# Performance work log

Hardware: AMD Instinct MI355X
Metric: run time of the kernel (lower is better)

## Reference

```python
import jax, jax.numpy as jnp
import numpy as np

B, I, O = 2048, 512, 512

def setup_inputs() -> dict:
    key = jax.random.key(0)
    kx, kw, ks = jax.random.split(key, 3)
    x = jax.random.uniform(kx, (B, I), dtype=jnp.float32)
    # shift weight logits so sigmoid(w) ~ 0.02: keeps the length-I product
    # of implication factors away from underflow (sparse conjunction)
    w_logits = jax.random.normal(kw, (I, O), dtype=jnp.float32) - 4.0
    s_logits = jax.random.normal(ks, (I, O), dtype=jnp.float32)
    return {"x": x, "w_logits": w_logits, "s_logits": s_logits}

def reference(x, w_logits, s_logits):
    # FuzzyParam.value(): sigmoid of stored logits
    w = jax.nn.sigmoid(w_logits)   # (I, O)
    s = jax.nn.sigmoid(s_logits)   # (I, O)
    xi = x[:, :, None]             # (B, I, 1)
    # product fuzzy logic:
    #   bin_xnor(a, b) = a*b + (1-a)*(1-b)
    #   implies(a, b)  = 1 - a*(1 - b)
    #   conjoin        = prod along axis
    xnor = xi * s + (1.0 - xi) * (1.0 - s)      # (B, I, O)
    factors = 1.0 - w * (1.0 - xnor)            # (B, I, O)
    return jnp.prod(factors, axis=1)            # (B, O)
```

## Files before the change

kernel.cpp:

```cpp
#include <hip/hip_runtime.h>
#include <hip/hip_bf16.h>
#include <math.h>

#define B_DIM 2048
#define I_DIM 512
#define O_DIM 512

constexpr int R_ROWS  = 8;
constexpr int W_CHUNK = 4;
constexpr int CHUNK   = I_DIM / W_CHUNK;
constexpr int KP      = CHUNK / 2;
constexpr int QUADS   = I_DIM / 4;

#define XT_BYTES  ((size_t)B_DIM * I_DIM * 4)
#define AB_OFFSET XT_BYTES

__global__ __launch_bounds__(256) void setup_kernel(
    const float* __restrict__ x,
    const float* __restrict__ w_logits,
    const float* __restrict__ s_logits,
    float4* __restrict__ ab4,
    float4* __restrict__ xt4)
{
    const int blk = blockIdx.x;
    if (blk < 512) {
        int t = blk * 256 + threadIdx.x;
        int o  = t & (O_DIM - 1);
        int k  = t >> 9;
        int i0 = 2 * k;

        float zw0 = w_logits[(i0 + 0) * O_DIM + o];
        float zs0 = s_logits[(i0 + 0) * O_DIM + o];
        float zw1 = w_logits[(i0 + 1) * O_DIM + o];
        float zs1 = s_logits[(i0 + 1) * O_DIM + o];

        float w0 = 1.0f / (1.0f + expf(-zw0));
        float s0 = 1.0f / (1.0f + expf(-zs0));
        float w1 = 1.0f / (1.0f + expf(-zw1));
        float s1 = 1.0f / (1.0f + expf(-zs1));

        float4 v;
        v.x = fmaf(-w0, s0, 1.0f);
        v.y = fmaf(-w1, s1, 1.0f);
        v.z = w0 * (2.0f * s0 - 1.0f);
        v.w = w1 * (2.0f * s1 - 1.0f);
        ab4[k * O_DIM + o] = v;
    } else {
        int t  = (blk - 512) * 256 + threadIdx.x;
        int q  = t & (QUADS - 1);
        int b  = t >> 7;
        float4 v = ((const float4*)x)[(size_t)b * QUADS + q];
        xt4[((size_t)(b >> 3) * QUADS + q) * R_ROWS + (b & 7)] = v;
    }
}

__global__ __launch_bounds__(1024, 8) void fuzzy_main(
    const float4* __restrict__ xt,
    const float4* __restrict__ ab4,
    float* __restrict__ out)
{
    __shared__ float part[W_CHUNK][R_ROWS][256];

    const int o_l = threadIdx.x;
    const int o   = blockIdx.x * 256 + o_l;
    const int y   = __builtin_amdgcn_readfirstlane((int)threadIdx.y);
    const int g   = blockIdx.y;
    const int b0  = g * R_ROWS;
    const int kbase = y * KP;

    const float4* ab_o = ab4 + o;
    const float4* xq = xt + ((size_t)g * QUADS + (size_t)y * (KP / 2)) * R_ROWS;

    float4 xa[R_ROWS], xb[R_ROWS];
#pragma unroll
    for (int r = 0; r < R_ROWS; ++r) xa[r] = xq[r];
#pragma unroll
    for (int r = 0; r < R_ROWS; ++r) xb[r] = xq[R_ROWS + r];

    float4 pA0 = ab_o[(size_t)(kbase + 0) * O_DIM];
    float4 pA1 = ab_o[(size_t)(kbase + 1) * O_DIM];
    float4 pB0 = ab_o[(size_t)(kbase + 2) * O_DIM];
    float4 pB1 = ab_o[(size_t)(kbase + 3) * O_DIM];

    float acc0[R_ROWS], acc1[R_ROWS];
#pragma unroll
    for (int r = 0; r < R_ROWS; ++r) { acc0[r] = 1.0f; acc1[r] = 1.0f; }

    for (int k = 0; k < KP; k += 4) {
        {
            float4 c0 = pA0, c1 = pA1;
#pragma unroll
            for (int r = 0; r < R_ROWS; ++r) {
                float4 xv = xa[r];
                float f0 = fmaf(c0.z, xv.x, c0.x);
                float f1 = fmaf(c0.w, xv.y, c0.y);
                float f2 = fmaf(c1.z, xv.z, c1.x);
                float f3 = fmaf(c1.w, xv.w, c1.y);
                acc0[r] *= f0 * f2;
                acc1[r] *= f1 * f3;
            }
            pA0 = ab_o[(size_t)(kbase + k + 4) * O_DIM];
            pA1 = ab_o[(size_t)(kbase + k + 5) * O_DIM];
            const float4* xs = xq + (size_t)(k / 2 + 2) * R_ROWS;
#pragma unroll
            for (int r = 0; r < R_ROWS; ++r) xa[r] = xs[r];
        }
        {
            float4 c0 = pB0, c1 = pB1;
#pragma unroll
            for (int r = 0; r < R_ROWS; ++r) {
                float4 xv = xb[r];
                float f0 = fmaf(c0.z, xv.x, c0.x);
                float f1 = fmaf(c0.w, xv.y, c0.y);
                float f2 = fmaf(c1.z, xv.z, c1.x);
                float f3 = fmaf(c1.w, xv.w, c1.y);
                acc0[r] *= f0 * f2;
                acc1[r] *= f1 * f3;
            }
            pB0 = ab_o[(size_t)(kbase + k + 6) * O_DIM];
            pB1 = ab_o[(size_t)(kbase + k + 7) * O_DIM];
            const float4* xs = xq + (size_t)(k / 2 + 3) * R_ROWS;
#pragma unroll
            for (int r = 0; r < R_ROWS; ++r) xb[r] = xs[r];
        }
    }

#pragma unroll
    for (int r = 0; r < R_ROWS; ++r)
        part[y][r][o_l] = acc0[r] * acc1[r];
    __syncthreads();
#pragma unroll
    for (int rr = 0; rr < 2; ++rr) {
        int r8 = y * 2 + rr;
        float v = part[0][r8][o_l] * part[1][r8][o_l]
                * part[2][r8][o_l] * part[3][r8][o_l];
        out[(size_t)(b0 + r8) * O_DIM + o] = v;
    }
}

extern "C" void kernel_launch(void* const* d_in, const int* in_sizes, int n_in,
                              void* d_out, int out_size, void* d_ws, size_t ws_size,
                              hipStream_t stream) {
    const float* x        = (const float*)d_in[0];
    const float* w_logits = (const float*)d_in[1];
    const float* s_logits = (const float*)d_in[2];
    float* out = (float*)d_out;
    float4* xt4 = (float4*)d_ws;
    float4* ab4 = (float4*)((char*)d_ws + AB_OFFSET);

    setup_kernel<<<dim3(1536), dim3(256), 0, stream>>>(
        x, w_logits, s_logits, ab4, xt4);

    fuzzy_main<<<dim3(O_DIM / 256, B_DIM / R_ROWS), dim3(256, W_CHUNK), 0, stream>>>(
        xt4, ab4, out);
}
```

Baseline: 92.73 us.

## Stage x rows in LDS and double rows per block, drop x transpose pass

Removes the x-transpose half of the setup kernel and instead has each block cooperatively load its 16 rows of x into shared memory, which is then reused for the final partial-product reduction. Rows per block go from 8 to 16, halving the grid and doubling reuse of each loaded weight-coefficient vector. The two accumulators per row are merged into one. This trades a global transpose pass and per-thread register-held x for LDS broadcast reads plus an extra barrier, with lower occupancy hints.

```diff
diff --git a/kernel.cpp b/kernel.cpp
--- a/kernel.cpp
+++ b/kernel.cpp
@@ -1,65 +1,52 @@
 #include <hip/hip_runtime.h>
-#include <hip/hip_bf16.h>
 #include <math.h>
 
 #define B_DIM 2048
 #define I_DIM 512
 #define O_DIM 512
 
-constexpr int R_ROWS  = 8;
+constexpr int R_ROWS  = 16;
 constexpr int W_CHUNK = 4;
 constexpr int CHUNK   = I_DIM / W_CHUNK;
 constexpr int KP      = CHUNK / 2;
-constexpr int QUADS   = I_DIM / 4;
 
-#define XT_BYTES  ((size_t)B_DIM * I_DIM * 4)
-#define AB_OFFSET XT_BYTES
 
 __global__ __launch_bounds__(256) void setup_kernel(
-    const float* __restrict__ x,
     const float* __restrict__ w_logits,
     const float* __restrict__ s_logits,
-    float4* __restrict__ ab4,
-    float4* __restrict__ xt4)
+    float4* __restrict__ ab4)
 {
-    const int blk = blockIdx.x;
-    if (blk < 512) {
-        int t = blk * 256 + threadIdx.x;
-        int o  = t & (O_DIM - 1);
-        int k  = t >> 9;
-        int i0 = 2 * k;
+    int t  = blockIdx.x * 256 + threadIdx.x;
+    int o  = t & (O_DIM - 1);
+    int k  = t >> 9;
+    int i0 = 2 * k;
 
-        float zw0 = w_logits[(i0 + 0) * O_DIM + o];
-        float zs0 = s_logits[(i0 + 0) * O_DIM + o];
-        float zw1 = w_logits[(i0 + 1) * O_DIM + o];
-        float zs1 = s_logits[(i0 + 1) * O_DIM + o];
+    float zw0 = w_logits[(i0 + 0) * O_DIM + o];
+    float zs0 = s_logits[(i0 + 0) * O_DIM + o];
+    float zw1 = w_logits[(i0 + 1) * O_DIM + o];
+    float zs1 = s_logits[(i0 + 1) * O_DIM + o];
 
-        float w0 = 1.0f / (1.0f + expf(-zw0));
-        float s0 = 1.0f / (1.0f + expf(-zs0));
-        float w1 = 1.0f / (1.0f + expf(-zw1));
-        float s1 = 1.0f / (1.0f + expf(-zs1));
+    float w0 = 1.0f / (1.0f + expf(-zw0));
+    float s0 = 1.0f / (1.0f + expf(-zs0));
+    float w1 = 1.0f / (1.0f + expf(-zw1));
+    float s1 = 1.0f / (1.0f + expf(-zs1));
 
-        float4 v;
-        v.x = fmaf(-w0, s0, 1.0f);
-        v.y = fmaf(-w1, s1, 1.0f);
-        v.z = w0 * (2.0f * s0 - 1.0f);
-        v.w = w1 * (2.0f * s1 - 1.0f);
-        ab4[k * O_DIM + o] = v;
-    } else {
-        int t  = (blk - 512) * 256 + threadIdx.x;
-        int q  = t & (QUADS - 1);
-        int b  = t >> 7;
-        float4 v = ((const float4*)x)[(size_t)b * QUADS + q];
-        xt4[((size_t)(b >> 3) * QUADS + q) * R_ROWS + (b & 7)] = v;
-    }
+    float4 v;
+    v.x = fmaf(-w0, s0, 1.0f);
+    v.y = fmaf(-w1, s1, 1.0f);
+    v.z = w0 * (2.0f * s0 - 1.0f);
+    v.w = w1 * (2.0f * s1 - 1.0f);
+    ab4[k * O_DIM + o] = v;
 }
 
-__global__ __launch_bounds__(1024, 8) void fuzzy_main(
-    const float4* __restrict__ xt,
+__global__ __launch_bounds__(1024, 4) void fuzzy_main(
+    const float* __restrict__ x,
     const float4* __restrict__ ab4,
     float* __restrict__ out)
 {
-    __shared__ float part[W_CHUNK][R_ROWS][256];
+    __shared__ __align__(16) unsigned char sh_raw[W_CHUNK * R_ROWS * 256 * 4];
+    float4 (*xs4)[CHUNK]        = reinterpret_cast<float4(*)[CHUNK]>(sh_raw);
+    float  (*part)[R_ROWS][256] = reinterpret_cast<float(*)[R_ROWS][256]>(sh_raw);
 
     const int o_l = threadIdx.x;
     const int o   = blockIdx.x * 256 + o_l;
@@ -69,72 +56,72 @@
     const int kbase = y * KP;
 
     const float4* ab_o = ab4 + o;
-    const float4* xq = xt + ((size_t)g * QUADS + (size_t)y * (KP / 2)) * R_ROWS;
-
-    float4 xa[R_ROWS], xb[R_ROWS];
-#pragma unroll
-    for (int r = 0; r < R_ROWS; ++r) xa[r] = xq[r];
-#pragma unroll
-    for (int r = 0; r < R_ROWS; ++r) xb[r] = xq[R_ROWS + r];
 
     float4 pA0 = ab_o[(size_t)(kbase + 0) * O_DIM];
     float4 pA1 = ab_o[(size_t)(kbase + 1) * O_DIM];
     float4 pB0 = ab_o[(size_t)(kbase + 2) * O_DIM];
     float4 pB1 = ab_o[(size_t)(kbase + 3) * O_DIM];
 
-    float acc0[R_ROWS], acc1[R_ROWS];
+    {
+        const float4* x4 = (const float4*)x;
+        const int tid = threadIdx.y * 256 + o_l;
 #pragma unroll
-    for (int r = 0; r < R_ROWS; ++r) { acc0[r] = 1.0f; acc1[r] = 1.0f; }
+        for (int p = 0; p < 2; ++p) {
+            int fidx = p * 1024 + tid;
+            int r = fidx >> 7;
+            int q = fidx & (CHUNK - 1);
+            xs4[r][q] = x4[(size_t)(b0 + r) * (I_DIM / 4) + q];
+        }
+    }
+    __syncthreads();
+
+    float acc[R_ROWS];
+#pragma unroll
+    for (int r = 0; r < R_ROWS; ++r) acc[r] = 1.0f;
 
     for (int k = 0; k < KP; k += 4) {
+        const int qA = (kbase + k) >> 1;
         {
             float4 c0 = pA0, c1 = pA1;
+            pA0 = ab_o[(size_t)(kbase + k + 4) * O_DIM];
+            pA1 = ab_o[(size_t)(kbase + k + 5) * O_DIM];
 #pragma unroll
             for (int r = 0; r < R_ROWS; ++r) {
-                float4 xv = xa[r];
+                float4 xv = xs4[r][qA];
                 float f0 = fmaf(c0.z, xv.x, c0.x);
                 float f1 = fmaf(c0.w, xv.y, c0.y);
                 float f2 = fmaf(c1.z, xv.z, c1.x);
                 float f3 = fmaf(c1.w, xv.w, c1.y);
-                acc0[r] *= f0 * f2;
-                acc1[r] *= f1 * f3;
+                acc[r] *= (f0 * f2) * (f1 * f3);
             }
-            pA0 = ab_o[(size_t)(kbase + k + 4) * O_DIM];
-            pA1 = ab_o[(size_t)(kbase + k + 5) * O_DIM];
-            const float4* xs = xq + (size_t)(k / 2 + 2) * R_ROWS;
-#pragma unroll
-            for (int r = 0; r < R_ROWS; ++r) xa[r] = xs[r];
         }
         {
             float4 c0 = pB0, c1 = pB1;
+            pB0 = ab_o[(size_t)(kbase + k + 6) * O_DIM];
+            pB1 = ab_o[(size_t)(kbase + k + 7) * O_DIM];
 #pragma unroll
             for (int r = 0; r < R_ROWS; ++r) {
-                float4 xv = xb[r];
+                float4 xv = xs4[r][qA + 1];
                 float f0 = fmaf(c0.z, xv.x, c0.x);
                 float f1 = fmaf(c0.w, xv.y, c0.y);
                 float f2 = fmaf(c1.z, xv.z, c1.x);
                 float f3 = fmaf(c1.w, xv.w, c1.y);
-                acc0[r] *= f0 * f2;
-                acc1[r] *= f1 * f3;
+                acc[r] *= (f0 * f2) * (f1 * f3);
             }
-            pB0 = ab_o[(size_t)(kbase + k + 6) * O_DIM];
-            pB1 = ab_o[(size_t)(kbase + k + 7) * O_DIM];
-            const float4* xs = xq + (size_t)(k / 2 + 3) * R_ROWS;
-#pragma unroll
-            for (int r = 0; r < R_ROWS; ++r) xb[r] = xs[r];
         }
     }
 
+    __syncthreads();
 #pragma unroll
     for (int r = 0; r < R_ROWS; ++r)
-        part[y][r][o_l] = acc0[r] * acc1[r];
+        part[y][r][o_l] = acc[r];
     __syncthreads();
 #pragma unroll
-    for (int rr = 0; rr < 2; ++rr) {
-        int r8 = y * 2 + rr;
-        float v = part[0][r8][o_l] * part[1][r8][o_l]
-                * part[2][r8][o_l] * part[3][r8][o_l];
-        out[(size_t)(b0 + r8) * O_DIM + o] = v;
+    for (int rr = 0; rr < 4; ++rr) {
+        int r = y * 4 + rr;
+        float v = part[0][r][o_l] * part[1][r][o_l]
+                * part[2][r][o_l] * part[3][r][o_l];
+        out[(size_t)(b0 + r) * O_DIM + o] = v;
     }
 }
 
@@ -145,12 +132,10 @@
     const float* w_logits = (const float*)d_in[1];
     const float* s_logits = (const float*)d_in[2];
     float* out = (float*)d_out;
-    float4* xt4 = (float4*)d_ws;
-    float4* ab4 = (float4*)((char*)d_ws + AB_OFFSET);
+    float4* ab4 = (float4*)d_ws;
 
-    setup_kernel<<<dim3(1536), dim3(256), 0, stream>>>(
-        x, w_logits, s_logits, ab4, xt4);
+    setup_kernel<<<dim3(512), dim3(256), 0, stream>>>(w_logits, s_logits, ab4);
 
     fuzzy_main<<<dim3(O_DIM / 256, B_DIM / R_ROWS), dim3(256, W_CHUNK), 0, stream>>>(
-        xt4, ab4, out);
+        x, ab4, out);
 }
```

Result: slower. 97.91 us (+5.6%).
